# Performance work log

Measured on AMD Instinct MI355X. Metric: run time of the kernel, lower is better.

## Reference

```python
import math
import jax, jax.numpy as jnp
import numpy as np


def _shapley_tables(L):
    """Static subset-lattice tables for L views.

    masks: [M, L] 0/1 membership of view l in subset m (M = 2^L).
    coef:  [L, M] Shapley combination coefficients so that
           shapley[l] = sum_m coef[l, m] * relu(Linear(sum_{j in m} feats[j])).
    Derivation (faithful to the torch loops): for view i and every nonempty
    subset S not containing i, contrib = f(sum_{S u {i}}) - f(feats_i) with
    weight |S|! (L-|S|-1)! / L!, plus f(feats_i)/L.  Letting T = S u {i}
    (|T| >= 2, i in T) and noting sum of weights over all S is (L-1)/L and
    f(feats_i) = f(sum over singleton {i}):
      coef[i, T]          = (|T|-1)! (L-|T|)! / L!   for |T|>=2, i in T
      coef[i, {i}]       += -(L-1)/L + 1/L = -(L-2)/L
    """
    M = 1 << L
    fact = math.factorial
    masks = np.zeros((M, L), np.float32)
    coef = np.zeros((L, M), np.float32)
    for m in range(M):
        bits = [i for i in range(L) if (m >> i) & 1]
        for i in bits:
            masks[m, i] = 1.0
        t = len(bits)
        if t >= 2:
            wgt = fact(t - 1) * fact(L - t) / fact(L)
            for i in bits:
                coef[i, m] += wgt
    for i in range(L):
        coef[i, 1 << i] += -(L - 2) / L
    return jnp.asarray(masks), jnp.asarray(coef)


def setup_inputs() -> dict:
    key = jax.random.key(0)
    k1, k2 = jax.random.split(key)
    L, C, H, W = 5, 64, 128, 256
    feats = jax.random.normal(k1, (L, C, H, W), dtype=jnp.float32)
    w = jax.random.normal(k2, (C, 1), dtype=jnp.float32) / np.sqrt(C)
    b = jnp.zeros((1,), dtype=jnp.float32)
    return {"feats": feats, "w": w, "b": b}


def reference(feats, w, b):
    L, C, H, W = feats.shape
    N = H * W
    masks, coef = _shapley_tables(L)
    x = feats.reshape(L, C, N).transpose(0, 2, 1)          # [L, N, C]
    # all 2^L subset sums in one GEMM over the (tiny) L axis
    subset_sums = jnp.einsum('ml,lnc->mnc', masks, x)       # [M, N, C]
    f_sums = jax.nn.relu(subset_sums @ w + b)               # [M, N, 1]
    shapley = jnp.einsum('lm,mnj->lnj', coef, f_sums)       # [L, N, 1]
    attn = jax.nn.softmax(shapley, axis=0)                  # softmax over views
    fused = jnp.sum(x * attn, axis=0)                       # [N, C]
    return fused.T.reshape(C, H, W)
```

## Files before the change

### kernel.cpp

```cpp
#include <hip/hip_runtime.h>


constexpr int L_VIEWS = 5;
constexpr int C_CH    = 64;
constexpr int NPIX    = 128 * 256;

__global__ __launch_bounds__(256)
void shapley_fusion_kernel(const float* __restrict__ feats,
                           const float* __restrict__ w,
                           const float* __restrict__ bptr,
                           float* __restrict__ out)
{
    const int lane = threadIdx.x & 63;
    const int wid  = threadIdx.x >> 6;
    const int n4l  = lane & 3;
    const int cg   = lane >> 2;
    const int n    = (blockIdx.x * 4 + wid) * 16 + n4l * 4;
    const int c0   = cg * 4;

    const float4 wv  = *reinterpret_cast<const float4*>(w + c0);
    const float bias = bptr[0];

    float4 v[L_VIEWS][4];
#pragma unroll
    for (int l = 0; l < L_VIEWS; ++l)
#pragma unroll
        for (int cc = 0; cc < 4; ++cc)
            v[l][cc] = *reinterpret_cast<const float4*>(
                feats + ((size_t)(l * C_CH + c0 + cc) * NPIX + n));

    float d[L_VIEWS][4];
#pragma unroll
    for (int l = 0; l < L_VIEWS; ++l) {
        d[l][0] = v[l][0].x * wv.x + v[l][1].x * wv.y + v[l][2].x * wv.z + v[l][3].x * wv.w;
        d[l][1] = v[l][0].y * wv.x + v[l][1].y * wv.y + v[l][2].y * wv.z + v[l][3].y * wv.w;
        d[l][2] = v[l][0].z * wv.x + v[l][1].z * wv.y + v[l][2].z * wv.z + v[l][3].z * wv.w;
        d[l][3] = v[l][0].w * wv.x + v[l][1].w * wv.y + v[l][2].w * wv.z + v[l][3].w * wv.w;
    }

#pragma unroll
    for (int l = 0; l < L_VIEWS; ++l) {
#pragma unroll
        for (int j = 0; j < 4; ++j) {
            d[l][j] += __shfl_xor(d[l][j], 4, 64);
            d[l][j] += __shfl_xor(d[l][j], 8, 64);
            d[l][j] += __shfl_xor(d[l][j], 16, 64);
            d[l][j] += __shfl_xor(d[l][j], 32, 64);
        }
    }

    constexpr float WT1 = -0.6f;
    constexpr float WT2 = 0.05f;
    constexpr float WT3 = 1.0f / 30.0f;
    constexpr float WT4 = 0.05f;
    constexpr float WT5 = 0.2f;

    float attn[L_VIEWS][4];
#pragma unroll
    for (int j = 0; j < 4; ++j) {
        float s[32];
        s[0] = 0.f;
        float sh[L_VIEWS] = {0.f, 0.f, 0.f, 0.f, 0.f};
#pragma unroll
        for (int m = 1; m < 32; ++m) {
            const int lb  = m & (-m);
            const int lbi = __builtin_ctz(m);
            s[m] = s[m ^ lb] + d[lbi][j];
            const float f = fmaxf(s[m] + bias, 0.f);
            const int pc = __builtin_popcount(m);
            const float wt = (pc == 1) ? WT1 : (pc == 2) ? WT2
                           : (pc == 3) ? WT3 : (pc == 4) ? WT4 : WT5;
#pragma unroll
            for (int i = 0; i < L_VIEWS; ++i)
                if (m & (1 << i)) sh[i] += wt * f;
        }
        float mx = sh[0];
#pragma unroll
        for (int i = 1; i < L_VIEWS; ++i) mx = fmaxf(mx, sh[i]);
        float e[L_VIEWS];
        float sum = 0.f;
#pragma unroll
        for (int i = 0; i < L_VIEWS; ++i) { e[i] = __expf(sh[i] - mx); sum += e[i]; }
        const float inv = 1.f / sum;
#pragma unroll
        for (int i = 0; i < L_VIEWS; ++i) attn[i][j] = e[i] * inv;
    }

#pragma unroll
    for (int cc = 0; cc < 4; ++cc) {
        float4 acc;
        acc.x = v[0][cc].x * attn[0][0];
        acc.y = v[0][cc].y * attn[0][1];
        acc.z = v[0][cc].z * attn[0][2];
        acc.w = v[0][cc].w * attn[0][3];
#pragma unroll
        for (int l = 1; l < L_VIEWS; ++l) {
            acc.x += v[l][cc].x * attn[l][0];
            acc.y += v[l][cc].y * attn[l][1];
            acc.z += v[l][cc].z * attn[l][2];
            acc.w += v[l][cc].w * attn[l][3];
        }
        *reinterpret_cast<float4*>(out + (size_t)(c0 + cc) * NPIX + n) = acc;
    }
}

extern "C" void kernel_launch(void* const* d_in, const int* in_sizes, int n_in,
                              void* d_out, int out_size, void* d_ws, size_t ws_size,
                              hipStream_t stream) {
    const float* feats = (const float*)d_in[0];
    const float* w     = (const float*)d_in[1];
    const float* b     = (const float*)d_in[2];
    float* out         = (float*)d_out;

    shapley_fusion_kernel<<<NPIX / 64, 256, 0, stream>>>(feats, w, b, out);
}
```

Baseline: 16.70 us.

## Split channels across two waves per pixel group and reload feats for the output

Each 16-pixel group is now handled by a 128-thread block of two wavefronts, each covering 32 channels (2 per lane) instead of one wave covering all 64. The two partial dot products are combined through shared memory with a block barrier, and the feature tile is reloaded from global memory (expected to hit cache) for the weighted sum instead of being held in registers. This lowers registers per thread and raises the block count and occupancy to hide memory latency better. The cost is a __syncthreads, the shared-memory exchange, a second round of loads, and the Shapley/softmax math now being done redundantly by both waves.

```diff
diff --git a/kernel.cpp b/kernel.cpp
--- a/kernel.cpp
+++ b/kernel.cpp
@@ -5,37 +5,39 @@
 constexpr int C_CH    = 64;
 constexpr int NPIX    = 128 * 256;
 
-__global__ __launch_bounds__(256)
+__global__ __launch_bounds__(128, 4)
 void shapley_fusion_kernel(const float* __restrict__ feats,
                            const float* __restrict__ w,
                            const float* __restrict__ bptr,
                            float* __restrict__ out)
 {
-    const int lane = threadIdx.x & 63;
-    const int wid  = threadIdx.x >> 6;
+    const int tid  = threadIdx.x;
+    const int h    = tid >> 6;
+    const int lane = tid & 63;
     const int n4l  = lane & 3;
     const int cg   = lane >> 2;
-    const int n    = (blockIdx.x * 4 + wid) * 16 + n4l * 4;
-    const int c0   = cg * 4;
+    const int n    = blockIdx.x * 16 + n4l * 4;
+    const int c0   = h * 32 + cg * 2;
 
-    const float4 wv  = *reinterpret_cast<const float4*>(w + c0);
+    const float w0   = w[c0];
+    const float w1   = w[c0 + 1];
     const float bias = bptr[0];
 
-    float4 v[L_VIEWS][4];
+    float4 va[L_VIEWS][2];
 #pragma unroll
     for (int l = 0; l < L_VIEWS; ++l)
 #pragma unroll
-        for (int cc = 0; cc < 4; ++cc)
-            v[l][cc] = *reinterpret_cast<const float4*>(
+        for (int cc = 0; cc < 2; ++cc)
+            va[l][cc] = *reinterpret_cast<const float4*>(
                 feats + ((size_t)(l * C_CH + c0 + cc) * NPIX + n));
 
     float d[L_VIEWS][4];
 #pragma unroll
     for (int l = 0; l < L_VIEWS; ++l) {
-        d[l][0] = v[l][0].x * wv.x + v[l][1].x * wv.y + v[l][2].x * wv.z + v[l][3].x * wv.w;
-        d[l][1] = v[l][0].y * wv.x + v[l][1].y * wv.y + v[l][2].y * wv.z + v[l][3].y * wv.w;
-        d[l][2] = v[l][0].z * wv.x + v[l][1].z * wv.y + v[l][2].z * wv.z + v[l][3].z * wv.w;
-        d[l][3] = v[l][0].w * wv.x + v[l][1].w * wv.y + v[l][2].w * wv.z + v[l][3].w * wv.w;
+        d[l][0] = va[l][0].x * w0 + va[l][1].x * w1;
+        d[l][1] = va[l][0].y * w0 + va[l][1].y * w1;
+        d[l][2] = va[l][0].z * w0 + va[l][1].z * w1;
+        d[l][3] = va[l][0].w * w0 + va[l][1].w * w1;
     }
 
 #pragma unroll
@@ -49,6 +51,21 @@
         }
     }
 
+    __shared__ float xl[2 * 4 * L_VIEWS * 4];
+    if (cg == 0) {
+#pragma unroll
+        for (int l = 0; l < L_VIEWS; ++l)
+#pragma unroll
+            for (int j = 0; j < 4; ++j)
+                xl[((h * 4 + n4l) * L_VIEWS + l) * 4 + j] = d[l][j];
+    }
+    __syncthreads();
+#pragma unroll
+    for (int l = 0; l < L_VIEWS; ++l)
+#pragma unroll
+        for (int j = 0; j < 4; ++j)
+            d[l][j] += xl[(((1 - h) * 4 + n4l) * L_VIEWS + l) * 4 + j];
+
     constexpr float WT1 = -0.6f;
     constexpr float WT2 = 0.05f;
     constexpr float WT3 = 1.0f / 30.0f;
@@ -59,14 +76,14 @@
 #pragma unroll
     for (int j = 0; j < 4; ++j) {
         float s[32];
-        s[0] = 0.f;
+        s[0] = bias;
         float sh[L_VIEWS] = {0.f, 0.f, 0.f, 0.f, 0.f};
 #pragma unroll
         for (int m = 1; m < 32; ++m) {
             const int lb  = m & (-m);
             const int lbi = __builtin_ctz(m);
             s[m] = s[m ^ lb] + d[lbi][j];
-            const float f = fmaxf(s[m] + bias, 0.f);
+            const float f = fmaxf(s[m], 0.f);
             const int pc = __builtin_popcount(m);
             const float wt = (pc == 1) ? WT1 : (pc == 2) ? WT2
                            : (pc == 3) ? WT3 : (pc == 4) ? WT4 : WT5;
@@ -81,24 +98,32 @@
         float sum = 0.f;
 #pragma unroll
         for (int i = 0; i < L_VIEWS; ++i) { e[i] = __expf(sh[i] - mx); sum += e[i]; }
-        const float inv = 1.f / sum;
+        const float inv = __fdividef(1.f, sum);
 #pragma unroll
         for (int i = 0; i < L_VIEWS; ++i) attn[i][j] = e[i] * inv;
     }
 
+    float4 vc[L_VIEWS][2];
 #pragma unroll
-    for (int cc = 0; cc < 4; ++cc) {
+    for (int l = 0; l < L_VIEWS; ++l)
+#pragma unroll
+        for (int cc = 0; cc < 2; ++cc)
+            vc[l][cc] = *reinterpret_cast<const float4*>(
+                feats + ((size_t)(l * C_CH + c0 + cc) * NPIX + n));
+
+#pragma unroll
+    for (int cc = 0; cc < 2; ++cc) {
         float4 acc;
-        acc.x = v[0][cc].x * attn[0][0];
-        acc.y = v[0][cc].y * attn[0][1];
-        acc.z = v[0][cc].z * attn[0][2];
-        acc.w = v[0][cc].w * attn[0][3];
+        acc.x = vc[0][cc].x * attn[0][0];
+        acc.y = vc[0][cc].y * attn[0][1];
+        acc.z = vc[0][cc].z * attn[0][2];
+        acc.w = vc[0][cc].w * attn[0][3];
 #pragma unroll
         for (int l = 1; l < L_VIEWS; ++l) {
-            acc.x += v[l][cc].x * attn[l][0];
-            acc.y += v[l][cc].y * attn[l][1];
-            acc.z += v[l][cc].z * attn[l][2];
-            acc.w += v[l][cc].w * attn[l][3];
+            acc.x += vc[l][cc].x * attn[l][0];
+            acc.y += vc[l][cc].y * attn[l][1];
+            acc.z += vc[l][cc].z * attn[l][2];
+            acc.w += vc[l][cc].w * attn[l][3];
         }
         *reinterpret_cast<float4*>(out + (size_t)(c0 + cc) * NPIX + n) = acc;
     }
@@ -112,5 +137,5 @@
     const float* b     = (const float*)d_in[2];
     float* out         = (float*)d_out;
 
-    shapley_fusion_kernel<<<NPIX / 64, 256, 0, stream>>>(feats, w, b, out);
+    shapley_fusion_kernel<<<NPIX / 16, 128, 0, stream>>>(feats, w, b, out);
 }
```

After: 32.30 us. 1.93x slower.
